# Performance work log

Measured on AMD Instinct MI355X. Metric: run time of the kernel, lower is better.

## Reference

```python
import jax, jax.numpy as jnp
import numpy as np

T_STEPS = 16
A = 64
B = 64
N = 16          # read_N
C = 3           # channels
H = 1024        # enc_size
IN = N * N * C  # LSTM input size = 768
EPS = 1e-8


def setup_inputs() -> dict:
    key = jax.random.key(0)
    ks = jax.random.split(key, 12)
    s = 0.02
    x = jax.random.normal(ks[0], (1024, C, B, A), dtype=jnp.float32)
    W_att = jax.random.normal(ks[1], (5, H), dtype=jnp.float32) * s
    b_att = jnp.zeros((5,), dtype=jnp.float32)
    W_ih = jax.random.normal(ks[2], (4 * H, IN), dtype=jnp.float32) * s
    W_hh = jax.random.normal(ks[3], (4 * H, H), dtype=jnp.float32) * s
    b_ih = jnp.zeros((4 * H,), dtype=jnp.float32)
    b_hh = jnp.zeros((4 * H,), dtype=jnp.float32)
    W_fc0 = jax.random.normal(ks[4], (H, H), dtype=jnp.float32) * s
    b_fc0 = jnp.zeros((H,), dtype=jnp.float32)
    W_fc = jax.random.normal(ks[5], (10, H), dtype=jnp.float32) * s
    b_fc = jnp.zeros((10,), dtype=jnp.float32)
    return {"x": x, "W_att": W_att, "b_att": b_att, "W_ih": W_ih, "W_hh": W_hh,
            "b_ih": b_ih, "b_hh": b_hh, "W_fc0": W_fc0, "b_fc0": b_fc0,
            "W_fc": W_fc, "b_fc": b_fc}


def _filterbank(gx, gy, sigma2, delta):
    # gx, gy, sigma2, delta: [Bt]
    grid = jnp.arange(N, dtype=jnp.float32)
    mu_x = gx[:, None] + (grid - N / 2 - 0.5) * delta[:, None]   # [Bt, N]
    mu_y = gy[:, None] + (grid - N / 2 - 0.5) * delta[:, None]   # [Bt, N]
    a = jnp.arange(A, dtype=jnp.float32)
    b = jnp.arange(B, dtype=jnp.float32)
    s2 = sigma2[:, None, None]
    Fx = jnp.exp(-(a[None, None, :] - mu_x[:, :, None]) ** 2 / (2 * s2))  # [Bt,N,A]
    Fy = jnp.exp(-(b[None, None, :] - mu_y[:, :, None]) ** 2 / (2 * s2))  # [Bt,N,B]
    Fx = Fx / (Fx.sum(2, keepdims=True) + EPS)
    Fy = Fy / (Fy.sum(2, keepdims=True) + EPS)
    return Fx, Fy


def _forward(x, W_att, b_att, W_ih, W_hh, b_ih, b_hh, W_fc0, b_fc0, W_fc, b_fc):
    Bt = x.shape[0]
    img = x.reshape(Bt, C, B, A)
    h0 = jnp.zeros((Bt, H), dtype=x.dtype)
    c0 = jnp.zeros((Bt, H), dtype=x.dtype)

    def step(carry, _):
        h, c = carry
        p = h @ W_att.T + b_att                      # [Bt, 5]
        gx_, gy_, log_s2, log_d, log_g = (p[:, 0], p[:, 1], p[:, 2], p[:, 3], p[:, 4])
        gx = (A + 1) / 2 * (gx_ + 1)
        gy = (B + 1) / 2 * (gy_ + 1)
        delta = (max(A, B) - 1) / (N - 1) * jnp.exp(log_d)
        sigma2 = jnp.exp(log_s2)
        gamma = jnp.exp(log_g)
        Fx, Fy = _filterbank(gx, gy, sigma2, delta)
        # glimpse[b,c] = Fy @ img[b,c] @ Fx^T -> [Bt, C, N, N]
        glimpse = jnp.einsum('bny,bcya,bxa->bcnx', Fy, img, Fx)
        r = glimpse.reshape(Bt, IN) * gamma[:, None]
        gates = r @ W_ih.T + b_ih + h @ W_hh.T + b_hh
        i_g, f_g, g_g, o_g = jnp.split(gates, 4, axis=1)
        c_new = jax.nn.sigmoid(f_g) * c + jax.nn.sigmoid(i_g) * jnp.tanh(g_g)
        h_new = jax.nn.sigmoid(o_g) * jnp.tanh(c_new)
        return (h_new, c_new), None

    (h, _), _ = jax.lax.scan(step, (h0, c0), None, length=T_STEPS)
    t = jax.nn.relu(h @ W_fc0.T + b_fc0)
    return t @ W_fc.T + b_fc


def reference(x, W_att, b_att, W_ih, W_hh, b_ih, b_hh, W_fc0, b_fc0, W_fc, b_fc):
    return _forward(x, W_att, b_att, W_ih, W_hh, b_ih, b_hh, W_fc0, b_fc0, W_fc, b_fc)
```

## Files before the change

### kernel.cpp

```cpp
#include <hip/hip_runtime.h>

typedef unsigned short u16;
typedef unsigned int u32;
typedef _Float16 f16;
typedef _Float16 half8 __attribute__((ext_vector_type(8)));
typedef _Float16 half4 __attribute__((ext_vector_type(4)));
typedef float f32x4 __attribute__((ext_vector_type(4)));

#define SPLIT_SC 2048.0f
#define SPLIT_INV (1.0f / 2048.0f)

__device__ __forceinline__ float sigf(float x) { return 1.0f / (1.0f + expf(-x)); }

__global__ __launch_bounds__(256) void att_glimpse(
    const f16* __restrict__ h_hi, const f16* __restrict__ h_lo,
    const float* __restrict__ Watt, const float* __restrict__ batt,
    const float* __restrict__ x,
    f16* __restrict__ r_hi, f16* __restrict__ r_lo)
{
    __shared__ float simg[64 * 64];
    __shared__ float sFx[16 * 68];
    __shared__ float sFyT[64 * 20];
    __shared__ float stmp[16 * 68];
    __shared__ float sred[4 * 5];
    __shared__ float spar[8];

    const int b = blockIdx.x, c = blockIdx.y, tid = threadIdx.x;
    const int lane = tid & 63, wave = tid >> 6;

    {
        const float4* src = (const float4*)(x + (size_t)b * 12288 + c * 4096);
        float4* dst = (float4*)simg;
        for (int i = tid; i < 1024; i += 256) dst[i] = src[i];
    }

    float p[5] = {0.f, 0.f, 0.f, 0.f, 0.f};
    {
        const f16* hh = h_hi + (size_t)b * 1024;
        const f16* hl = h_lo + (size_t)b * 1024;
        for (int k = tid; k < 1024; k += 256) {
            float hv = (float)hh[k] + (float)hl[k] * SPLIT_INV;
#pragma unroll
            for (int j = 0; j < 5; j++) p[j] += hv * Watt[j * 1024 + k];
        }
#pragma unroll
        for (int j = 0; j < 5; j++) {
#pragma unroll
            for (int o = 32; o > 0; o >>= 1) p[j] += __shfl_xor(p[j], o);
        }
        if (lane == 0) {
#pragma unroll
            for (int j = 0; j < 5; j++) sred[wave * 5 + j] = p[j];
        }
    }
    __syncthreads();
    if (tid == 0) {
        float q[5];
#pragma unroll
        for (int j = 0; j < 5; j++)
            q[j] = sred[j] + sred[5 + j] + sred[10 + j] + sred[15 + j] + batt[j];
        float q2 = fminf(fmaxf(q[2], -60.f), 60.f);
        float q3 = fminf(fmaxf(q[3], -60.f), 60.f);
        float q4 = fminf(fmaxf(q[4], -60.f), 60.f);
        spar[0] = 32.5f * (q[0] + 1.0f);
        spar[1] = 32.5f * (q[1] + 1.0f);
        spar[2] = 0.5f * expf(-q2);
        spar[3] = 4.2f * expf(q3);
        spar[4] = expf(q4);
    }
    __syncthreads();
    const float gx = spar[0], gy = spar[1], inv2s2 = spar[2], dl = spar[3],
                gamma = spar[4];

    {
        const float af = (float)lane;
#pragma unroll
        for (int i = 0; i < 4; i++) {
            int n = wave + i * 4;
            float nn = (float)n - 8.5f;
            float mux = gx + nn * dl;
            float ex = af - mux;
            float vx = expf(-ex * ex * inv2s2);
            float sx = vx;
#pragma unroll
            for (int o = 32; o > 0; o >>= 1) sx += __shfl_xor(sx, o);
            sFx[n * 68 + lane] = vx / (sx + 1e-8f);

            float muy = gy + nn * dl;
            float ey = af - muy;
            float vy = expf(-ey * ey * inv2s2);
            float sy = vy;
#pragma unroll
            for (int o = 32; o > 0; o >>= 1) sy += __shfl_xor(sy, o);
            sFyT[lane * 20 + n] = vy / (sy + 1e-8f);
        }
    }
    __syncthreads();

    {
        const int n4 = wave, ysub = lane >> 4, a4 = lane & 15;
        f32x4 acc[4];
#pragma unroll
        for (int j = 0; j < 4; j++) acc[j] = (f32x4)(0.f);
        for (int yy = 0; yy < 16; yy++) {
            int y = ysub * 16 + yy;
            float4 im = *(const float4*)(simg + y * 64 + a4 * 4);
            float4 fy = *(const float4*)(sFyT + y * 20 + n4 * 4);
            f32x4 iv = {im.x, im.y, im.z, im.w};
            acc[0] += fy.x * iv;
            acc[1] += fy.y * iv;
            acc[2] += fy.z * iv;
            acc[3] += fy.w * iv;
        }
#pragma unroll
        for (int j = 0; j < 4; j++) {
#pragma unroll
            for (int o = 16; o <= 32; o <<= 1) {
                acc[j].x += __shfl_xor(acc[j].x, o);
                acc[j].y += __shfl_xor(acc[j].y, o);
                acc[j].z += __shfl_xor(acc[j].z, o);
                acc[j].w += __shfl_xor(acc[j].w, o);
            }
        }
        if (ysub == 0) {
#pragma unroll
            for (int j = 0; j < 4; j++)
                *(f32x4*)(stmp + (n4 * 4 + j) * 68 + a4 * 4) = acc[j];
        }
    }
    __syncthreads();

    {
        const int n = tid >> 4, xo = tid & 15;
        const float* tp = stmp + n * 68;
        const float* fx = sFx + xo * 68;
        float s = 0.f;
        for (int a = 0; a < 64; a += 4) {
            float4 t4 = *(const float4*)(tp + a);
            float4 x4 = *(const float4*)(fx + a);
            s += t4.x * x4.x + t4.y * x4.y + t4.z * x4.z + t4.w * x4.w;
        }
        float v = s * gamma;
        f16 hi = (f16)v;
        size_t idx = (size_t)b * 768 + c * 256 + tid;
        r_hi[idx] = hi;
        r_lo[idx] = (f16)((v - (float)hi) * SPLIT_SC);
    }
}

__global__ __launch_bounds__(256) void swz_w(
    const float* __restrict__ W1, const float* __restrict__ W2,
    f16* __restrict__ out)
{
    const int kc = blockIdx.x >> 5, bn = blockIdx.x & 31;
    for (int t = threadIdx.x; t < 512; t += 256) {
        int c = t >> 6, lane = t & 63, l15 = lane & 15, lq = lane >> 4;
        int gate = ((c & 1) << 1) + (l15 >> 3);
        int ul   = ((c >> 1) << 3) + (l15 & 7);
        int wrow = gate * 1024 + bn * 32 + ul;
        const float* src;
        if (kc < 24) src = W1 + (size_t)wrow * 768 + kc * 32 + lq * 8;
        else         src = W2 + (size_t)wrow * 1024 + (kc - 24) * 32 + lq * 8;
        float4 g0 = *(const float4*)src;
        float4 g1 = *(const float4*)(src + 4);
        float gv[8] = {g0.x, g0.y, g0.z, g0.w, g1.x, g1.y, g1.z, g1.w};
        half8 hv, lv;
#pragma unroll
        for (int j = 0; j < 8; j++) {
            f16 h = (f16)gv[j];
            hv[j] = h;
            lv[j] = (f16)((gv[j] - (float)h) * SPLIT_SC);
        }
        size_t base = ((size_t)(kc * 32 + bn) * 16 + c * 2) * 512 + (size_t)lane * 8;
        *(half8*)(out + base) = hv;
        *(half8*)(out + base + 512) = lv;
    }
}

#define LDH 40

__global__ __launch_bounds__(256, 2) void gates_lstm(
    const f16* __restrict__ A1h, const f16* __restrict__ A1l,
    const f16* __restrict__ A2h, const f16* __restrict__ A2l,
    const f16* __restrict__ Wswz,
    const float* __restrict__ b1, const float* __restrict__ b2,
    float* __restrict__ cst,
    f16* __restrict__ Hh, f16* __restrict__ Hl)
{
    __shared__ f16 sA[2][2][64 * LDH];
    const int tid = threadIdx.x;
    const int kb = blockIdx.x;
    const int xcd = kb & 7, jb = kb >> 3;
    const int bn = xcd * 4 + (jb & 3);
    const int bm = jb >> 2;
    const int wave = tid >> 6, lane = tid & 63;
    const int cbase = wave * 2;
    const int l15 = lane & 15, lq = lane >> 4;
    const int arow = tid >> 2, acol = (tid & 3) * 8;

    f32x4 ah[4][2], al[4][2];
#pragma unroll
    for (int i = 0; i < 4; i++)
#pragma unroll
        for (int j = 0; j < 2; j++) { ah[i][j] = (f32x4)(0.f); al[i][j] = (f32x4)(0.f); }

    {
        size_t aoff = (size_t)(bm * 64 + arow) * 768 + acol;
        *(uint4*)&sA[0][0][arow * LDH + acol] = *(const uint4*)(A1h + aoff);
        *(uint4*)&sA[0][1][arow * LDH + acol] = *(const uint4*)(A1l + aoff);
    }
    half8 Bc[4];
    {
        const f16* wb = Wswz + (size_t)bn * 16 * 512 + (size_t)lane * 8;
#pragma unroll
        for (int nt = 0; nt < 2; nt++) {
            Bc[nt * 2]     = *(const half8*)(wb + (cbase + nt) * 1024);
            Bc[nt * 2 + 1] = *(const half8*)(wb + (cbase + nt) * 1024 + 512);
        }
    }

#pragma unroll 2
    for (int i = 0; i < 56; ++i) {
        const int cur = i & 1;
        __syncthreads();
        const int kn = (i + 1 < 56) ? i + 1 : 55;
        const f16 *pah, *pal; int astr, ako;
        if (kn < 24) { pah = A1h; pal = A1l; astr = 768;  ako = kn * 32; }
        else         { pah = A2h; pal = A2l; astr = 1024; ako = (kn - 24) * 32; }
        size_t aoff = (size_t)(bm * 64 + arow) * astr + ako + acol;
        uint4 vh = *(const uint4*)(pah + aoff);
        uint4 vl = *(const uint4*)(pal + aoff);
        half8 Bn[4];
        {
            const f16* wb = Wswz + (size_t)(kn * 32 + bn) * 16 * 512 + (size_t)lane * 8;
#pragma unroll
            for (int nt = 0; nt < 2; nt++) {
                Bn[nt * 2]     = *(const half8*)(wb + (cbase + nt) * 1024);
                Bn[nt * 2 + 1] = *(const half8*)(wb + (cbase + nt) * 1024 + 512);
            }
        }
        half8 afh[4], afl[4];
#pragma unroll
        for (int mt = 0; mt < 4; mt++) {
            int ro = (mt * 16 + l15) * LDH + lq * 8;
            afh[mt] = *(const half8*)&sA[cur][0][ro];
            afl[mt] = *(const half8*)&sA[cur][1][ro];
        }
#pragma unroll
        for (int mt = 0; mt < 4; mt++)
#pragma unroll
            for (int nt = 0; nt < 2; nt++) {
                ah[mt][nt] = __builtin_amdgcn_mfma_f32_16x16x32_f16(
                    afh[mt], Bc[nt * 2], ah[mt][nt], 0, 0, 0);
                al[mt][nt] = __builtin_amdgcn_mfma_f32_16x16x32_f16(
                    afh[mt], Bc[nt * 2 + 1], al[mt][nt], 0, 0, 0);
                al[mt][nt] = __builtin_amdgcn_mfma_f32_16x16x32_f16(
                    afl[mt], Bc[nt * 2], al[mt][nt], 0, 0, 0);
            }
        const int nxt = cur ^ 1;
        *(uint4*)&sA[nxt][0][arow * LDH + acol] = vh;
        *(uint4*)&sA[nxt][1][arow * LDH + acol] = vl;
#pragma unroll
        for (int q = 0; q < 4; q++) Bc[q] = Bn[q];
    }

    const int g0 = l15 >> 3;
    const int u = bn * 32 + wave * 8 + (l15 & 7);
    const float bv0 = b1[g0 * 1024 + u] + b2[g0 * 1024 + u];
    const float bv1 = b1[(g0 + 2) * 1024 + u] + b2[(g0 + 2) * 1024 + u];
#pragma unroll
    for (int mt = 0; mt < 4; mt++) {
#pragma unroll
        for (int rg = 0; rg < 4; rg++) {
            int row = bm * 64 + mt * 16 + lq * 4 + rg;
            size_t idx = (size_t)row * 1024 + u;
            float mine0 = ah[mt][0][rg] + al[mt][0][rg] * SPLIT_INV + bv0;
            float mine1 = ah[mt][1][rg] + al[mt][1][rg] * SPLIT_INV + bv1;
            float oth0 = __shfl_xor(mine0, 8);
            float oth1 = __shfl_xor(mine1, 8);
            float gi = (g0 == 0) ? mine0 : oth0;
            float gg = (g0 == 0) ? mine1 : oth1;
            float gf = (g0 == 0) ? oth0 : mine0;
            float go = (g0 == 0) ? oth1 : mine1;
            if (g0 == 0) {
                float cn = sigf(gf) * cst[idx] + sigf(gi) * tanhf(gg);
                float hn = sigf(go) * tanhf(cn);
                cst[idx] = cn;
                f16 hh = (f16)hn;
                Hh[idx] = hh;
                Hl[idx] = (f16)((hn - (float)hh) * SPLIT_SC);
            }
        }
    }
}

__global__ __launch_bounds__(256) void fc0_gemm(
    const f16* __restrict__ Ah, const f16* __restrict__ Al,
    const float* __restrict__ W, const float* __restrict__ bias,
    float* __restrict__ out)
{
    __shared__ f16 sAh[64 * LDH], sAl[64 * LDH];
    __shared__ f16 sBh[64 * LDH], sBl[64 * LDH];
    const int tid = threadIdx.x;
    const int bm = blockIdx.x, bn = blockIdx.y;
    const int wave = tid >> 6, lane = tid & 63;
    const int wm = (wave >> 1) * 32, wn = (wave & 1) * 32;
    const int l15 = lane & 15, lq = lane >> 4;

    f32x4 ach[2][2], acx[2][2];
#pragma unroll
    for (int i = 0; i < 2; i++)
#pragma unroll
        for (int j = 0; j < 2; j++) { ach[i][j] = (f32x4)(0.f); acx[i][j] = (f32x4)(0.f); }

    for (int kc = 0; kc < 1024; kc += 32) {
        {
            int e = tid * 8;
            int row = e >> 5, col = e & 31;
            size_t off = (size_t)(bm * 64 + row) * 1024 + kc + col;
            *(uint4*)&sAh[row * LDH + col] = *(const uint4*)(Ah + off);
            *(uint4*)&sAl[row * LDH + col] = *(const uint4*)(Al + off);
        }
#pragma unroll
        for (int l = 0; l < 2; l++) {
            int e = (l * 256 + tid) * 4;
            int crow = e >> 5, col = e & 31;
            float4 g = *(const float4*)(W + (size_t)(bn * 64 + crow) * 1024 + kc + col);
            f16 h0 = (f16)g.x, h1 = (f16)g.y, h2 = (f16)g.z, h3 = (f16)g.w;
            half4 hv = {h0, h1, h2, h3};
            half4 lv = {(f16)((g.x - (float)h0) * SPLIT_SC),
                        (f16)((g.y - (float)h1) * SPLIT_SC),
                        (f16)((g.z - (float)h2) * SPLIT_SC),
                        (f16)((g.w - (float)h3) * SPLIT_SC)};
            *(half4*)&sBh[crow * LDH + col] = hv;
            *(half4*)&sBl[crow * LDH + col] = lv;
        }
        __syncthreads();
        half8 afh[2], afl[2], bfh[2], bfl[2];
#pragma unroll
        for (int mt = 0; mt < 2; mt++) {
            int ro = (wm + mt * 16 + l15) * LDH + lq * 8;
            afh[mt] = *(const half8*)&sAh[ro];
            afl[mt] = *(const half8*)&sAl[ro];
        }
#pragma unroll
        for (int nt = 0; nt < 2; nt++) {
            int ro = (wn + nt * 16 + l15) * LDH + lq * 8;
            bfh[nt] = *(const half8*)&sBh[ro];
            bfl[nt] = *(const half8*)&sBl[ro];
        }
#pragma unroll
        for (int mt = 0; mt < 2; mt++)
#pragma unroll
            for (int nt = 0; nt < 2; nt++) {
                ach[mt][nt] = __builtin_amdgcn_mfma_f32_16x16x32_f16(
                    afh[mt], bfh[nt], ach[mt][nt], 0, 0, 0);
                acx[mt][nt] = __builtin_amdgcn_mfma_f32_16x16x32_f16(
                    afh[mt], bfl[nt], acx[mt][nt], 0, 0, 0);
                acx[mt][nt] = __builtin_amdgcn_mfma_f32_16x16x32_f16(
                    afl[mt], bfh[nt], acx[mt][nt], 0, 0, 0);
            }
        __syncthreads();
    }

#pragma unroll
    for (int mt = 0; mt < 2; mt++) {
#pragma unroll
        for (int nt = 0; nt < 2; nt++) {
            int col = bn * 64 + wn + nt * 16 + l15;
            float bv = bias[col];
#pragma unroll
            for (int rg = 0; rg < 4; rg++) {
                int row = bm * 64 + wm + mt * 16 + lq * 4 + rg;
                float v = ach[mt][nt][rg] + acx[mt][nt][rg] * SPLIT_INV + bv;
                out[(size_t)row * 1024 + col] = fmaxf(v, 0.f);
            }
        }
    }
}

__global__ __launch_bounds__(64) void fc_out(
    const float* __restrict__ tb, const float* __restrict__ Wfc,
    const float* __restrict__ bfc, float* __restrict__ out)
{
    int b = blockIdx.x, lane = threadIdx.x;
    const float* tv = tb + (size_t)b * 1024;
    float p[10];
#pragma unroll
    for (int j = 0; j < 10; j++) p[j] = 0.f;
    for (int k = lane; k < 1024; k += 64) {
        float t = tv[k];
#pragma unroll
        for (int j = 0; j < 10; j++) p[j] += t * Wfc[j * 1024 + k];
    }
#pragma unroll
    for (int j = 0; j < 10; j++) {
#pragma unroll
        for (int o = 32; o > 0; o >>= 1) p[j] += __shfl_xor(p[j], o);
    }
    if (lane == 0) {
#pragma unroll
        for (int j = 0; j < 10; j++) out[b * 10 + j] = p[j] + bfc[j];
    }
}

extern "C" void kernel_launch(void* const* d_in, const int* in_sizes, int n_in,
                              void* d_out, int out_size, void* d_ws, size_t ws_size,
                              hipStream_t stream)
{
    const float* x     = (const float*)d_in[0];
    const float* W_att = (const float*)d_in[1];
    const float* b_att = (const float*)d_in[2];
    const float* W_ih  = (const float*)d_in[3];
    const float* W_hh  = (const float*)d_in[4];
    const float* b_ih  = (const float*)d_in[5];
    const float* b_hh  = (const float*)d_in[6];
    const float* W_fc0 = (const float*)d_in[7];
    const float* b_fc0 = (const float*)d_in[8];
    const float* W_fc  = (const float*)d_in[9];
    const float* b_fc  = (const float*)d_in[10];
    float* out = (float*)d_out;

    char* ws = (char*)d_ws;
    f16*   Wswz   = (f16*)ws;    ws += (size_t)56 * 32 * 16 * 512 * 2;
    float* c_f32  = (float*)ws;  ws += (size_t)1024 * 1024 * 4;
    f16*   h_hi0  = (f16*)ws;    ws += (size_t)1024 * 1024 * 2;
    f16*   h_hi1  = (f16*)ws;    ws += (size_t)1024 * 1024 * 2;
    f16*   h_lo0  = (f16*)ws;    ws += (size_t)1024 * 1024 * 2;
    f16*   h_lo1  = (f16*)ws;    ws += (size_t)1024 * 1024 * 2;
    f16*   r_hi   = (f16*)ws;    ws += (size_t)1024 * 768 * 2;
    f16*   r_lo   = (f16*)ws;    ws += (size_t)1024 * 768 * 2;
    float* t_f32  = c_f32;
    f16* h_hi[2] = {h_hi0, h_hi1};
    f16* h_lo[2] = {h_lo0, h_lo1};

    hipMemsetAsync(c_f32, 0, (size_t)1024 * 1024 * 4, stream);
    hipMemsetAsync(h_hi0, 0, (size_t)1024 * 1024 * 2, stream);
    hipMemsetAsync(h_lo0, 0, (size_t)1024 * 1024 * 2, stream);

    swz_w<<<56 * 32, 256, 0, stream>>>(W_ih, W_hh, Wswz);

    for (int t = 0; t < 16; t++) {
        int rb = t & 1, wb = 1 - rb;
        att_glimpse<<<dim3(1024, 3), 256, 0, stream>>>(
            h_hi[rb], h_lo[rb], W_att, b_att, x, r_hi, r_lo);
        gates_lstm<<<512, 256, 0, stream>>>(
            r_hi, r_lo, h_hi[rb], h_lo[rb], Wswz, b_ih, b_hh,
            c_f32, h_hi[wb], h_lo[wb]);
    }
    fc0_gemm<<<dim3(16, 16), 256, 0, stream>>>(
        h_hi[0], h_lo[0], W_fc0, b_fc0, t_f32);
    fc_out<<<1024, 64, 0, stream>>>(t_f32, W_fc, b_fc, out);
}
```

Measured before the change: 1.464 ms.

## Store low-half activations in MFMA fragment order and load them directly to registers

The low-order f16 halves of the split-precision activations (r and h) are now written by producers in a pre-swizzled MFMA fragment layout. The gates GEMM and fc0 GEMM then load them straight from global memory into registers, prefetched one step ahead, instead of staging them through LDS. This halves the LDS traffic and shared-memory footprint for the A operand. The cost is scattered 2-byte stores from producers and a strided gather in att_glimpse.

```diff
diff --git a/kernel.cpp b/kernel.cpp
--- a/kernel.cpp
+++ b/kernel.cpp
@@ -12,11 +12,16 @@
 
 __device__ __forceinline__ float sigf(float x) { return 1.0f / (1.0f + expf(-x)); }
 
+__device__ __forceinline__ size_t fragA(int row, int k) {
+    return ((size_t)((k >> 5) * 64 + (row >> 4))) * 512
+         + (size_t)((((k & 31) >> 3) << 4) + (row & 15)) * 8 + (k & 7);
+}
+
 __global__ __launch_bounds__(256) void att_glimpse(
-    const f16* __restrict__ h_hi, const f16* __restrict__ h_lo,
+    const f16* __restrict__ h_hi, const f16* __restrict__ h_lof,
     const float* __restrict__ Watt, const float* __restrict__ batt,
     const float* __restrict__ x,
-    f16* __restrict__ r_hi, f16* __restrict__ r_lo)
+    f16* __restrict__ r_hi, f16* __restrict__ r_lof)
 {
     __shared__ float simg[64 * 64];
     __shared__ float sFx[16 * 68];
@@ -37,9 +42,8 @@
     float p[5] = {0.f, 0.f, 0.f, 0.f, 0.f};
     {
         const f16* hh = h_hi + (size_t)b * 1024;
-        const f16* hl = h_lo + (size_t)b * 1024;
         for (int k = tid; k < 1024; k += 256) {
-            float hv = (float)hh[k] + (float)hl[k] * SPLIT_INV;
+            float hv = (float)hh[k] + (float)h_lof[fragA(b, k)] * SPLIT_INV;
 #pragma unroll
             for (int j = 0; j < 5; j++) p[j] += hv * Watt[j * 1024 + k];
         }
@@ -142,9 +146,9 @@
         }
         float v = s * gamma;
         f16 hi = (f16)v;
-        size_t idx = (size_t)b * 768 + c * 256 + tid;
-        r_hi[idx] = hi;
-        r_lo[idx] = (f16)((v - (float)hi) * SPLIT_SC);
+        int k = c * 256 + tid;
+        r_hi[(size_t)b * 768 + k] = hi;
+        r_lof[fragA(b, k)] = (f16)((v - (float)hi) * SPLIT_SC);
     }
 }
 
@@ -180,14 +184,14 @@
 #define LDH 40
 
 __global__ __launch_bounds__(256, 2) void gates_lstm(
-    const f16* __restrict__ A1h, const f16* __restrict__ A1l,
-    const f16* __restrict__ A2h, const f16* __restrict__ A2l,
+    const f16* __restrict__ A1h, const f16* __restrict__ A1lf,
+    const f16* __restrict__ A2h, const f16* __restrict__ A2lf,
     const f16* __restrict__ Wswz,
     const float* __restrict__ b1, const float* __restrict__ b2,
     float* __restrict__ cst,
-    f16* __restrict__ Hh, f16* __restrict__ Hl)
-{
-    __shared__ f16 sA[2][2][64 * LDH];
+    f16* __restrict__ Hh, f16* __restrict__ Hlf)
+{
+    __shared__ f16 sA[2][64 * LDH];
     const int tid = threadIdx.x;
     const int kb = blockIdx.x;
     const int xcd = kb & 7, jb = kb >> 3;
@@ -206,10 +210,9 @@
 
     {
         size_t aoff = (size_t)(bm * 64 + arow) * 768 + acol;
-        *(uint4*)&sA[0][0][arow * LDH + acol] = *(const uint4*)(A1h + aoff);
-        *(uint4*)&sA[0][1][arow * LDH + acol] = *(const uint4*)(A1l + aoff);
-    }
-    half8 Bc[4];
+        *(uint4*)&sA[0][arow * LDH + acol] = *(const uint4*)(A1h + aoff);
+    }
+    half8 Bc[4], Alc[4];
     {
         const f16* wb = Wswz + (size_t)bn * 16 * 512 + (size_t)lane * 8;
 #pragma unroll
@@ -217,6 +220,10 @@
             Bc[nt * 2]     = *(const half8*)(wb + (cbase + nt) * 1024);
             Bc[nt * 2 + 1] = *(const half8*)(wb + (cbase + nt) * 1024 + 512);
         }
+        const f16* pa = A1lf + (size_t)(bm * 4) * 512 + (size_t)lane * 8;
+#pragma unroll
+        for (int mt = 0; mt < 4; mt++)
+            Alc[mt] = *(const half8*)(pa + mt * 512);
     }
 
 #pragma unroll 2
@@ -224,13 +231,14 @@
         const int cur = i & 1;
         __syncthreads();
         const int kn = (i + 1 < 56) ? i + 1 : 55;
-        const f16 *pah, *pal; int astr, ako;
-        if (kn < 24) { pah = A1h; pal = A1l; astr = 768;  ako = kn * 32; }
-        else         { pah = A2h; pal = A2l; astr = 1024; ako = (kn - 24) * 32; }
-        size_t aoff = (size_t)(bm * 64 + arow) * astr + ako + acol;
-        uint4 vh = *(const uint4*)(pah + aoff);
-        uint4 vl = *(const uint4*)(pal + aoff);
-        half8 Bn[4];
+        const f16 *pah; int astr, ako;
+        const f16 *palf; size_t abase;
+        if (kn < 24) { pah = A1h; astr = 768;  ako = kn * 32;
+                       palf = A1lf; abase = (size_t)(kn * 64 + bm * 4) * 512; }
+        else         { pah = A2h; astr = 1024; ako = (kn - 24) * 32;
+                       palf = A2lf; abase = (size_t)((kn - 24) * 64 + bm * 4) * 512; }
+        uint4 vh = *(const uint4*)(pah + (size_t)(bm * 64 + arow) * astr + ako + acol);
+        half8 Bn[4], Aln[4];
         {
             const f16* wb = Wswz + (size_t)(kn * 32 + bn) * 16 * 512 + (size_t)lane * 8;
 #pragma unroll
@@ -238,14 +246,15 @@
                 Bn[nt * 2]     = *(const half8*)(wb + (cbase + nt) * 1024);
                 Bn[nt * 2 + 1] = *(const half8*)(wb + (cbase + nt) * 1024 + 512);
             }
-        }
-        half8 afh[4], afl[4];
-#pragma unroll
-        for (int mt = 0; mt < 4; mt++) {
-            int ro = (mt * 16 + l15) * LDH + lq * 8;
-            afh[mt] = *(const half8*)&sA[cur][0][ro];
-            afl[mt] = *(const half8*)&sA[cur][1][ro];
-        }
+            const f16* pa = palf + (size_t)lane * 8;
+#pragma unroll
+            for (int mt = 0; mt < 4; mt++)
+                Aln[mt] = *(const half8*)(pa + abase + mt * 512);
+        }
+        half8 afh[4];
+#pragma unroll
+        for (int mt = 0; mt < 4; mt++)
+            afh[mt] = *(const half8*)&sA[cur][(mt * 16 + l15) * LDH + lq * 8];
 #pragma unroll
         for (int mt = 0; mt < 4; mt++)
 #pragma unroll
@@ -255,13 +264,12 @@
                 al[mt][nt] = __builtin_amdgcn_mfma_f32_16x16x32_f16(
                     afh[mt], Bc[nt * 2 + 1], al[mt][nt], 0, 0, 0);
                 al[mt][nt] = __builtin_amdgcn_mfma_f32_16x16x32_f16(
-                    afl[mt], Bc[nt * 2], al[mt][nt], 0, 0, 0);
+                    Alc[mt], Bc[nt * 2], al[mt][nt], 0, 0, 0);
             }
         const int nxt = cur ^ 1;
-        *(uint4*)&sA[nxt][0][arow * LDH + acol] = vh;
-        *(uint4*)&sA[nxt][1][arow * LDH + acol] = vl;
-#pragma unroll
-        for (int q = 0; q < 4; q++) Bc[q] = Bn[q];
+        *(uint4*)&sA[nxt][arow * LDH + acol] = vh;
+#pragma unroll
+        for (int q = 0; q < 4; q++) { Bc[q] = Bn[q]; Alc[q] = Aln[q]; }
     }
 
     const int g0 = l15 >> 3;
@@ -288,18 +296,18 @@
                 cst[idx] = cn;
                 f16 hh = (f16)hn;
                 Hh[idx] = hh;
-                Hl[idx] = (f16)((hn - (float)hh) * SPLIT_SC);
+                Hlf[fragA(row, u)] = (f16)((hn - (float)hh) * SPLIT_SC);
             }
         }
     }
 }
 
 __global__ __launch_bounds__(256) void fc0_gemm(
-    const f16* __restrict__ Ah, const f16* __restrict__ Al,
+    const f16* __restrict__ Ah, const f16* __restrict__ Alf,
     const float* __restrict__ W, const float* __restrict__ bias,
     float* __restrict__ out)
 {
-    __shared__ f16 sAh[64 * LDH], sAl[64 * LDH];
+    __shared__ f16 sAh[64 * LDH];
     __shared__ f16 sBh[64 * LDH], sBl[64 * LDH];
     const int tid = threadIdx.x;
     const int bm = blockIdx.x, bn = blockIdx.y;
@@ -319,7 +327,6 @@
             int row = e >> 5, col = e & 31;
             size_t off = (size_t)(bm * 64 + row) * 1024 + kc + col;
             *(uint4*)&sAh[row * LDH + col] = *(const uint4*)(Ah + off);
-            *(uint4*)&sAl[row * LDH + col] = *(const uint4*)(Al + off);
         }
 #pragma unroll
         for (int l = 0; l < 2; l++) {
@@ -339,9 +346,10 @@
         half8 afh[2], afl[2], bfh[2], bfl[2];
 #pragma unroll
         for (int mt = 0; mt < 2; mt++) {
-            int ro = (wm + mt * 16 + l15) * LDH + lq * 8;
-            afh[mt] = *(const half8*)&sAh[ro];
-            afl[mt] = *(const half8*)&sAl[ro];
+            afh[mt] = *(const half8*)&sAh[(wm + mt * 16 + l15) * LDH + lq * 8];
+            int rt = bm * 4 + (wave >> 1) * 2 + mt;
+            afl[mt] = *(const half8*)(Alf + (size_t)((kc >> 5) * 64 + rt) * 512
+                                          + (size_t)lane * 8);
         }
 #pragma unroll
         for (int nt = 0; nt < 2; nt++) {
@@ -426,29 +434,29 @@
     float* c_f32  = (float*)ws;  ws += (size_t)1024 * 1024 * 4;
     f16*   h_hi0  = (f16*)ws;    ws += (size_t)1024 * 1024 * 2;
     f16*   h_hi1  = (f16*)ws;    ws += (size_t)1024 * 1024 * 2;
-    f16*   h_lo0  = (f16*)ws;    ws += (size_t)1024 * 1024 * 2;
-    f16*   h_lo1  = (f16*)ws;    ws += (size_t)1024 * 1024 * 2;
+    f16*   h_lof0 = (f16*)ws;    ws += (size_t)32 * 64 * 512 * 2;
+    f16*   h_lof1 = (f16*)ws;    ws += (size_t)32 * 64 * 512 * 2;
     f16*   r_hi   = (f16*)ws;    ws += (size_t)1024 * 768 * 2;
-    f16*   r_lo   = (f16*)ws;    ws += (size_t)1024 * 768 * 2;
+    f16*   r_lof  = (f16*)ws;    ws += (size_t)24 * 64 * 512 * 2;
     float* t_f32  = c_f32;
-    f16* h_hi[2] = {h_hi0, h_hi1};
-    f16* h_lo[2] = {h_lo0, h_lo1};
+    f16* h_hi[2]  = {h_hi0, h_hi1};
+    f16* h_lof[2] = {h_lof0, h_lof1};
 
     hipMemsetAsync(c_f32, 0, (size_t)1024 * 1024 * 4, stream);
     hipMemsetAsync(h_hi0, 0, (size_t)1024 * 1024 * 2, stream);
-    hipMemsetAsync(h_lo0, 0, (size_t)1024 * 1024 * 2, stream);
+    hipMemsetAsync(h_lof0, 0, (size_t)32 * 64 * 512 * 2, stream);
 
     swz_w<<<56 * 32, 256, 0, stream>>>(W_ih, W_hh, Wswz);
 
     for (int t = 0; t < 16; t++) {
         int rb = t & 1, wb = 1 - rb;
         att_glimpse<<<dim3(1024, 3), 256, 0, stream>>>(
-            h_hi[rb], h_lo[rb], W_att, b_att, x, r_hi, r_lo);
+            h_hi[rb], h_lof[rb], W_att, b_att, x, r_hi, r_lof);
         gates_lstm<<<512, 256, 0, stream>>>(
-            r_hi, r_lo, h_hi[rb], h_lo[rb], Wswz, b_ih, b_hh,
-            c_f32, h_hi[wb], h_lo[wb]);
+            r_hi, r_lof, h_hi[rb], h_lof[rb], Wswz, b_ih, b_hh,
+            c_f32, h_hi[wb], h_lof[wb]);
     }
     fc0_gemm<<<dim3(16, 16), 256, 0, stream>>>(
-        h_hi[0], h_lo[0], W_fc0, b_fc0, t_f32);
+        h_hi[0], h_lof[0], W_fc0, b_fc0, t_f32);
     fc_out<<<1024, 64, 0, stream>>>(t_f32, W_fc, b_fc, out);
 }
```

After: 1.586 ms. 1.08x slower.
